# Kernel optimization log

Hardware: AMD Instinct MI355X
Metric: run time of the kernel (lower is better)

The kernel has to match this reference:

```python
import jax, jax.numpy as jnp
import numpy as np

B, NUM, LENTH, AUX = 32, 64, 64, 64
SIZE, OUT = 256, 256
IN_G = (LENTH + 1) * 2 + AUX  # 194


def _linear_params(k, fan_in, fan_out):
    # torch nn.Linear default init: U(-1/sqrt(fan_in), 1/sqrt(fan_in))
    s = 1.0 / np.sqrt(fan_in)
    kw, kb = jax.random.split(k)
    W = jax.random.uniform(kw, (fan_in, fan_out), minval=-s, maxval=s, dtype=jnp.float32)
    b = jax.random.uniform(kb, (fan_out,), minval=-s, maxval=s, dtype=jnp.float32)
    return W, b


def setup_inputs() -> dict:
    key = jax.random.key(0)
    ks = jax.random.split(key, 8)
    inp = {"x_aux": jax.random.normal(ks[0], (B, NUM, LENTH + AUX), dtype=jnp.float32)}
    dims = [("g1", IN_G, SIZE), ("g2", SIZE, SIZE), ("g3", SIZE, SIZE), ("g4", SIZE, OUT),
            ("f1", OUT, SIZE), ("f2", SIZE, SIZE), ("f3", SIZE, OUT)]
    for k, (name, fi, fo) in zip(ks[1:], dims):
        W, b = _linear_params(k, fi, fo)
        inp[name + "_w"] = W
        inp[name + "_b"] = b
    return inp


def reference(x_aux, g1_w, g1_b, g2_w, g2_b, g3_w, g3_b, g4_w, g4_b,
              f1_w, f1_b, f2_w, f2_b, f3_w, f3_b):
    bsz = x_aux.shape[0]
    # coord feature = object index i
    coord = jnp.broadcast_to(
        jnp.arange(NUM, dtype=x_aux.dtype)[None, :, None], (bsz, NUM, 1))
    x = jnp.concatenate([x_aux[:, :, :LENTH], coord], axis=-1)      # [B, N, LENTH+1]
    xa = jnp.concatenate([x_aux, coord], axis=-1)                   # [B, N, LENTH+AUX+1]
    # all-pairs broadcast+concat -> [B, N, N, IN_G]
    x_i = jnp.broadcast_to(x[:, None, :, :], (bsz, NUM, NUM, LENTH + 1))
    x_j = jnp.broadcast_to(xa[:, :, None, :], (bsz, NUM, NUM, LENTH + AUX + 1))
    pairs = jnp.concatenate([x_i, x_j], axis=-1)
    # shared g-MLP over every pair
    h = jax.nn.relu(pairs @ g1_w + g1_b)
    h = jax.nn.relu(h @ g2_w + g2_b)
    h = jax.nn.relu(h @ g3_w + g3_b)
    h = jax.nn.relu(h @ g4_w + g4_b)
    # sum-pool over all N*N pairs -> [B, OUT]
    x_g = h.sum(axis=(1, 2))
    # f-MLP (dropout treated as identity / eval mode)
    x_f = jax.nn.relu(x_g @ f1_w + f1_b)
    x_f = jax.nn.relu(x_f @ f2_w + f2_b)
    return x_f @ f3_w + f3_b
```

## Files before the change

### kernel.cpp

```cpp
#include <hip/hip_runtime.h>

#define BATCH 32
#define NOBJ  64
#define PADK  264

typedef _Float16 f16x4 __attribute__((ext_vector_type(4)));
typedef _Float16 f16x8 __attribute__((ext_vector_type(8)));
typedef float    f32x4 __attribute__((ext_vector_type(4)));
typedef float    f32x16 __attribute__((ext_vector_type(16)));

__global__ __launch_bounds__(256) void prep_weights(
    const float* __restrict__ g1w, const float* __restrict__ g2w,
    const float* __restrict__ g3w, const float* __restrict__ g4w,
    _Float16* __restrict__ wtf, float* __restrict__ xg) {
  __shared__ _Float16 tile[256][33];
  const int blk = blockIdx.x;
  const int t = threadIdx.x;
  xg[blk * 256 + t] = 0.0f;

  const int l  = blk >> 3;
  const int nt = blk & 7;
  const float* src = (l == 0) ? g1w : (l == 1) ? g2w : (l == 2) ? g3w : g4w;

  const int nn = t & 31, kb = t >> 5;
#pragma unroll 4
  for (int pass = 0; pass < 32; ++pass) {
    int kn = pass * 8 + kb;
    int ok;
    if (l == 0) {
      if (kn < 64)        ok = kn;
      else if (kn < 192)  ok = kn + 1;
      else if (kn == 192) ok = 64;
      else if (kn == 193) ok = 193;
      else                ok = -1;
    } else {
      ok = kn;
    }
    float v = (ok >= 0) ? src[(size_t)ok * 256 + nt * 32 + nn] : 0.0f;
    tile[kn][nn] = (_Float16)v;
  }
  __syncthreads();

  const int lane = t & 63;
  const int nfrag = lane & 31;
  const int kbase = (lane >> 5) * 8;
  _Float16* dst = wtf + ((size_t)(l * 8 + nt) * 16) * 512;
#pragma unroll
  for (int q = 0; q < 4; ++q) {
    int kk = (t >> 6) + 4 * q;
    f16x8 fr;
#pragma unroll
    for (int j = 0; j < 8; ++j)
      fr[j] = tile[kk * 16 + kbase + j][nfrag];
    *(f16x8*)(dst + (size_t)kk * 512 + lane * 8) = fr;
  }
}

__global__ __launch_bounds__(256, 4) void g_mlp_pool(
    const float* __restrict__ x_aux,
    const _Float16* __restrict__ wtf,
    const float* __restrict__ g1b, const float* __restrict__ g2b,
    const float* __restrict__ g3b, const float* __restrict__ g4b,
    float* __restrict__ xg) {
  __shared__ _Float16 As[64][PADK];

  const int b = blockIdx.x >> 6;
  const int i = blockIdx.x & 63;
  const int t = threadIdx.x;

  {
    const float* xb = x_aux + (size_t)b * NOBJ * 128;
    {
      const int c4 = t & 15, r0 = t >> 4;
#pragma unroll
      for (int it = 0; it < 4; ++it) {
        int r = it * 16 + r0;
        f32x4 v = *(const f32x4*)(xb + (size_t)r * 128 + c4 * 4);
        f16x4 hh = {(_Float16)v[0], (_Float16)v[1], (_Float16)v[2], (_Float16)v[3]};
        *(f16x4*)&As[r][c4 * 4] = hh;
      }
    }
    {
      const float* xi = xb + (size_t)i * 128;
      const int row = t >> 2, seg = t & 3;
#pragma unroll
      for (int u = 0; u < 4; ++u) {
        int c = seg * 32 + u * 8;
        f32x4 v0 = *(const f32x4*)(xi + c);
        f32x4 v1 = *(const f32x4*)(xi + c + 4);
        f16x8 hh = {(_Float16)v0[0], (_Float16)v0[1], (_Float16)v0[2], (_Float16)v0[3],
                    (_Float16)v1[0], (_Float16)v1[1], (_Float16)v1[2], (_Float16)v1[3]};
        *(f16x8*)&As[row][64 + c] = hh;
      }
      f16x8 z = {};
      *(f16x8*)&As[row][192 + seg * 16]     = z;
      *(f16x8*)&As[row][192 + seg * 16 + 8] = z;
      if (seg == 0) {
        As[row][192] = (_Float16)row;
        As[row][193] = (_Float16)i;
      }
    }
  }
  __syncthreads();

  const int lane = t & 63;
  const int wave = t >> 6;
  const int c31  = lane & 31;
  const int h    = lane >> 5;
  const int n0   = wave * 64;
  const float* gb[4] = {g1b, g2b, g3b, g4b};

  for (int layer = 0; layer < 4; ++layer) {
    const float bv0 = gb[layer][n0 + c31];
    const float bv1 = gb[layer][n0 + 32 + c31];

    f32x16 acc00 = {}, acc01 = {}, acc10 = {}, acc11 = {};

    const _Float16* bp0 =
        wtf + ((size_t)(layer * 8 + wave * 2) * 16) * 512 + lane * 8;
    const _Float16* bp1 = bp0 + 16 * 512;
    const _Float16* ar0 = &As[c31][h * 8];
    const _Float16* ar1 = &As[32 + c31][h * 8];

#pragma unroll
    for (int kk = 0; kk < 16; ++kk) {
      f16x8 b0 = *(const f16x8*)(bp0 + kk * 512);
      f16x8 b1 = *(const f16x8*)(bp1 + kk * 512);
      f16x8 a0 = *(const f16x8*)(ar0 + kk * 16);
      f16x8 a1 = *(const f16x8*)(ar1 + kk * 16);
      acc00 = __builtin_amdgcn_mfma_f32_32x32x16_f16(a0, b0, acc00, 0, 0, 0);
      acc10 = __builtin_amdgcn_mfma_f32_32x32x16_f16(a1, b0, acc10, 0, 0, 0);
      acc01 = __builtin_amdgcn_mfma_f32_32x32x16_f16(a0, b1, acc01, 0, 0, 0);
      acc11 = __builtin_amdgcn_mfma_f32_32x32x16_f16(a1, b1, acc11, 0, 0, 0);
    }

    if (layer < 3) {
      __syncthreads();
#pragma unroll
      for (int g = 0; g < 4; ++g)
#pragma unroll
        for (int r = 0; r < 4; ++r) {
          const int row = g * 8 + h * 4 + r;
          const int reg = g * 4 + r;
          As[row][n0 + c31]           = (_Float16)fmaxf(acc00[reg] + bv0, 0.f);
          As[32 + row][n0 + c31]      = (_Float16)fmaxf(acc10[reg] + bv0, 0.f);
          As[row][n0 + 32 + c31]      = (_Float16)fmaxf(acc01[reg] + bv1, 0.f);
          As[32 + row][n0 + 32 + c31] = (_Float16)fmaxf(acc11[reg] + bv1, 0.f);
        }
      __syncthreads();
    } else {
      float s0 = 0.f, s1 = 0.f;
#pragma unroll
      for (int reg = 0; reg < 16; ++reg) {
        s0 += fmaxf(acc00[reg] + bv0, 0.f) + fmaxf(acc10[reg] + bv0, 0.f);
        s1 += fmaxf(acc01[reg] + bv1, 0.f) + fmaxf(acc11[reg] + bv1, 0.f);
      }
      s0 += __shfl_xor(s0, 32, 64);
      s1 += __shfl_xor(s1, 32, 64);
      if (h == 0) {
        atomicAdd(&xg[b * 256 + n0 + c31], s0);
        atomicAdd(&xg[b * 256 + n0 + 32 + c31], s1);
      }
    }
  }
}

__global__ __launch_bounds__(1024) void f_mlp(
    const float* __restrict__ xg,
    const float* __restrict__ f1w, const float* __restrict__ f1b,
    const float* __restrict__ f2w, const float* __restrict__ f2b,
    const float* __restrict__ f3w, const float* __restrict__ f3b,
    float* __restrict__ out) {
  __shared__ float xs[256], ys[256], ps[4][256];
  const int b = blockIdx.x;
  const int t = threadIdx.x;
  const int n = t & 255;
  const int kc = t >> 8;

  if (t < 256) xs[t] = xg[b * 256 + t];
  __syncthreads();

  float p = 0.f;
#pragma unroll 8
  for (int k0 = 0; k0 < 64; ++k0) {
    int k = kc * 64 + k0;
    p += xs[k] * f1w[k * 256 + n];
  }
  ps[kc][n] = p;
  __syncthreads();
  if (t < 256)
    ys[t] = fmaxf(f1b[t] + ps[0][t] + ps[1][t] + ps[2][t] + ps[3][t], 0.f);
  __syncthreads();

  p = 0.f;
#pragma unroll 8
  for (int k0 = 0; k0 < 64; ++k0) {
    int k = kc * 64 + k0;
    p += ys[k] * f2w[k * 256 + n];
  }
  ps[kc][n] = p;
  __syncthreads();
  if (t < 256)
    xs[t] = fmaxf(f2b[t] + ps[0][t] + ps[1][t] + ps[2][t] + ps[3][t], 0.f);
  __syncthreads();

  p = 0.f;
#pragma unroll 8
  for (int k0 = 0; k0 < 64; ++k0) {
    int k = kc * 64 + k0;
    p += xs[k] * f3w[k * 256 + n];
  }
  ps[kc][n] = p;
  __syncthreads();
  if (t < 256)
    out[b * 256 + t] = f3b[t] + ps[0][t] + ps[1][t] + ps[2][t] + ps[3][t];
}

extern "C" void kernel_launch(void* const* d_in, const int* in_sizes, int n_in,
                              void* d_out, int out_size, void* d_ws, size_t ws_size,
                              hipStream_t stream) {
  const float* x_aux = (const float*)d_in[0];
  const float* g1w = (const float*)d_in[1];
  const float* g1b = (const float*)d_in[2];
  const float* g2w = (const float*)d_in[3];
  const float* g2b = (const float*)d_in[4];
  const float* g3w = (const float*)d_in[5];
  const float* g3b = (const float*)d_in[6];
  const float* g4w = (const float*)d_in[7];
  const float* g4b = (const float*)d_in[8];
  const float* f1w = (const float*)d_in[9];
  const float* f1b = (const float*)d_in[10];
  const float* f2w = (const float*)d_in[11];
  const float* f2b = (const float*)d_in[12];
  const float* f3w = (const float*)d_in[13];
  const float* f3b = (const float*)d_in[14];
  float* out = (float*)d_out;

  _Float16* wtf = (_Float16*)d_ws;
  float* xg = (float*)((char*)d_ws + 4u * 256u * 256u * 2u);

  hipLaunchKernelGGL(prep_weights, dim3(32), dim3(256), 0, stream,
                     g1w, g2w, g3w, g4w, wtf, xg);
  hipLaunchKernelGGL(g_mlp_pool, dim3(BATCH * NOBJ), dim3(256), 0, stream,
                     x_aux, wtf, g1b, g2b, g3b, g4b, xg);
  hipLaunchKernelGGL(f_mlp, dim3(BATCH), dim3(1024), 0, stream,
                     xg, f1w, f1b, f2w, f2b, f3w, f3b, out);
}
```

Measured before the change: 174.1 us.

## Process two object rows per block with 8 waves sharing weight fragments

Each workgroup now handles two i-values (128 pair rows) with 512 threads, and each wave computes a 128x32 output tile instead of 64x64. This halves the number of blocks and halves the global weight-fragment traffic per pair row, since each B fragment is reused across four A tiles. In exchange LDS use per block doubles to about 66KB, which limits occupancy, and the work per kernel becomes coarser, with 1024 blocks.

```diff
diff --git a/kernel.cpp b/kernel.cpp
--- a/kernel.cpp
+++ b/kernel.cpp
@@ -56,17 +56,17 @@
   }
 }
 
-__global__ __launch_bounds__(256, 4) void g_mlp_pool(
+__global__ __launch_bounds__(512, 4) void g_mlp_pool(
     const float* __restrict__ x_aux,
     const _Float16* __restrict__ wtf,
     const float* __restrict__ g1b, const float* __restrict__ g2b,
     const float* __restrict__ g3b, const float* __restrict__ g4b,
     float* __restrict__ xg) {
-  __shared__ _Float16 As[64][PADK];
-
-  const int b = blockIdx.x >> 6;
-  const int i = blockIdx.x & 63;
-  const int t = threadIdx.x;
+  __shared__ _Float16 As[128][PADK];
+
+  const int b  = blockIdx.x >> 5;
+  const int i0 = (blockIdx.x & 31) * 2;
+  const int t  = threadIdx.x;
 
   {
     const float* xb = x_aux + (size_t)b * NOBJ * 128;
@@ -74,15 +74,16 @@
       const int c4 = t & 15, r0 = t >> 4;
 #pragma unroll
       for (int it = 0; it < 4; ++it) {
-        int r = it * 16 + r0;
-        f32x4 v = *(const f32x4*)(xb + (size_t)r * 128 + c4 * 4);
+        int r = it * 32 + r0;
+        f32x4 v = *(const f32x4*)(xb + (size_t)(r & 63) * 128 + c4 * 4);
         f16x4 hh = {(_Float16)v[0], (_Float16)v[1], (_Float16)v[2], (_Float16)v[3]};
         *(f16x4*)&As[r][c4 * 4] = hh;
       }
     }
     {
-      const float* xi = xb + (size_t)i * 128;
       const int row = t >> 2, seg = t & 3;
+      const int ir = i0 + (row >> 6);
+      const float* xi = xb + (size_t)ir * 128;
 #pragma unroll
       for (int u = 0; u < 4; ++u) {
         int c = seg * 32 + u * 8;
@@ -96,8 +97,8 @@
       *(f16x8*)&As[row][192 + seg * 16]     = z;
       *(f16x8*)&As[row][192 + seg * 16 + 8] = z;
       if (seg == 0) {
-        As[row][192] = (_Float16)row;
-        As[row][193] = (_Float16)i;
+        As[row][192] = (_Float16)(row & 63);
+        As[row][193] = (_Float16)ir;
       }
     }
   }
@@ -107,31 +108,32 @@
   const int wave = t >> 6;
   const int c31  = lane & 31;
   const int h    = lane >> 5;
-  const int n0   = wave * 64;
+  const int n0   = wave * 32;
   const float* gb[4] = {g1b, g2b, g3b, g4b};
 
   for (int layer = 0; layer < 4; ++layer) {
-    const float bv0 = gb[layer][n0 + c31];
-    const float bv1 = gb[layer][n0 + 32 + c31];
-
-    f32x16 acc00 = {}, acc01 = {}, acc10 = {}, acc11 = {};
-
-    const _Float16* bp0 =
-        wtf + ((size_t)(layer * 8 + wave * 2) * 16) * 512 + lane * 8;
-    const _Float16* bp1 = bp0 + 16 * 512;
+    const float bv = gb[layer][n0 + c31];
+
+    f32x16 acc0 = {}, acc1 = {}, acc2 = {}, acc3 = {};
+
+    const _Float16* bp =
+        wtf + ((size_t)(layer * 8 + wave) * 16) * 512 + lane * 8;
     const _Float16* ar0 = &As[c31][h * 8];
     const _Float16* ar1 = &As[32 + c31][h * 8];
+    const _Float16* ar2 = &As[64 + c31][h * 8];
+    const _Float16* ar3 = &As[96 + c31][h * 8];
 
 #pragma unroll
     for (int kk = 0; kk < 16; ++kk) {
-      f16x8 b0 = *(const f16x8*)(bp0 + kk * 512);
-      f16x8 b1 = *(const f16x8*)(bp1 + kk * 512);
+      f16x8 bfr = *(const f16x8*)(bp + kk * 512);
       f16x8 a0 = *(const f16x8*)(ar0 + kk * 16);
       f16x8 a1 = *(const f16x8*)(ar1 + kk * 16);
-      acc00 = __builtin_amdgcn_mfma_f32_32x32x16_f16(a0, b0, acc00, 0, 0, 0);
-      acc10 = __builtin_amdgcn_mfma_f32_32x32x16_f16(a1, b0, acc10, 0, 0, 0);
-      acc01 = __builtin_amdgcn_mfma_f32_32x32x16_f16(a0, b1, acc01, 0, 0, 0);
-      acc11 = __builtin_amdgcn_mfma_f32_32x32x16_f16(a1, b1, acc11, 0, 0, 0);
+      f16x8 a2 = *(const f16x8*)(ar2 + kk * 16);
+      f16x8 a3 = *(const f16x8*)(ar3 + kk * 16);
+      acc0 = __builtin_amdgcn_mfma_f32_32x32x16_f16(a0, bfr, acc0, 0, 0, 0);
+      acc1 = __builtin_amdgcn_mfma_f32_32x32x16_f16(a1, bfr, acc1, 0, 0, 0);
+      acc2 = __builtin_amdgcn_mfma_f32_32x32x16_f16(a2, bfr, acc2, 0, 0, 0);
+      acc3 = __builtin_amdgcn_mfma_f32_32x32x16_f16(a3, bfr, acc3, 0, 0, 0);
     }
 
     if (layer < 3) {
@@ -142,25 +144,22 @@
         for (int r = 0; r < 4; ++r) {
           const int row = g * 8 + h * 4 + r;
           const int reg = g * 4 + r;
-          As[row][n0 + c31]           = (_Float16)fmaxf(acc00[reg] + bv0, 0.f);
-          As[32 + row][n0 + c31]      = (_Float16)fmaxf(acc10[reg] + bv0, 0.f);
-          As[row][n0 + 32 + c31]      = (_Float16)fmaxf(acc01[reg] + bv1, 0.f);
-          As[32 + row][n0 + 32 + c31] = (_Float16)fmaxf(acc11[reg] + bv1, 0.f);
+          As[row][n0 + c31]      = (_Float16)fmaxf(acc0[reg] + bv, 0.f);
+          As[32 + row][n0 + c31] = (_Float16)fmaxf(acc1[reg] + bv, 0.f);
+          As[64 + row][n0 + c31] = (_Float16)fmaxf(acc2[reg] + bv, 0.f);
+          As[96 + row][n0 + c31] = (_Float16)fmaxf(acc3[reg] + bv, 0.f);
         }
       __syncthreads();
     } else {
-      float s0 = 0.f, s1 = 0.f;
+      float s = 0.f;
 #pragma unroll
       for (int reg = 0; reg < 16; ++reg) {
-        s0 += fmaxf(acc00[reg] + bv0, 0.f) + fmaxf(acc10[reg] + bv0, 0.f);
-        s1 += fmaxf(acc01[reg] + bv1, 0.f) + fmaxf(acc11[reg] + bv1, 0.f);
-      }
-      s0 += __shfl_xor(s0, 32, 64);
-      s1 += __shfl_xor(s1, 32, 64);
-      if (h == 0) {
-        atomicAdd(&xg[b * 256 + n0 + c31], s0);
-        atomicAdd(&xg[b * 256 + n0 + 32 + c31], s1);
-      }
+        s += fmaxf(acc0[reg] + bv, 0.f) + fmaxf(acc1[reg] + bv, 0.f)
+           + fmaxf(acc2[reg] + bv, 0.f) + fmaxf(acc3[reg] + bv, 0.f);
+      }
+      s += __shfl_xor(s, 32, 64);
+      if (h == 0)
+        atomicAdd(&xg[b * 256 + n0 + c31], s);
     }
   }
 }
@@ -241,7 +240,7 @@
 
   hipLaunchKernelGGL(prep_weights, dim3(32), dim3(256), 0, stream,
                      g1w, g2w, g3w, g4w, wtf, xg);
-  hipLaunchKernelGGL(g_mlp_pool, dim3(BATCH * NOBJ), dim3(256), 0, stream,
+  hipLaunchKernelGGL(g_mlp_pool, dim3(BATCH * 32), dim3(512), 0, stream,
                      x_aux, wtf, g1b, g2b, g3b, g4b, xg);
   hipLaunchKernelGGL(f_mlp, dim3(BATCH), dim3(1024), 0, stream,
                      xg, f1w, f1b, f2w, f2b, f3w, f3b, out);
```

Result: faster. 168.9 us (-3.0%).

## Process two objects per block, prefetch B fragments, skip zero-padded K steps

Applied to the files above, without the earlier changes.

Each block now handles two i-objects (128 pair rows) with 512 threads. Two waves share each weight column slice, which halves per-block weight-fragment reuse overhead and the block count. The GEMM loop is factored into a helper that software-prefetches the next B fragment before issuing the MFMAs. The first layer runs only 13 K-steps because rows past 208 are zero padding. The larger LDS tile (128x264 halves) and bigger blocks may reduce occupancy.

```diff
diff --git a/kernel.cpp b/kernel.cpp
--- a/kernel.cpp
+++ b/kernel.cpp
@@ -8,6 +8,8 @@
 typedef _Float16 f16x8 __attribute__((ext_vector_type(8)));
 typedef float    f32x4 __attribute__((ext_vector_type(4)));
 typedef float    f32x16 __attribute__((ext_vector_type(16)));
+
+#define MFMA32(a, b, c) __builtin_amdgcn_mfma_f32_32x32x16_f16((a), (b), (c), 0, 0, 0)
 
 __global__ __launch_bounds__(256) void prep_weights(
     const float* __restrict__ g1w, const float* __restrict__ g2w,
@@ -56,17 +58,41 @@
   }
 }
 
-__global__ __launch_bounds__(256, 4) void g_mlp_pool(
+template <int STEPS>
+__device__ __forceinline__ void gemm_2x2(
+    const _Float16* bp0, const _Float16* bp1,
+    const _Float16* ar0, const _Float16* ar1,
+    f32x16& acc00, f32x16& acc10, f32x16& acc01, f32x16& acc11) {
+  f16x8 b0 = *(const f16x8*)bp0;
+  f16x8 b1 = *(const f16x8*)bp1;
+#pragma unroll
+  for (int kk = 0; kk < STEPS; ++kk) {
+    f16x8 a0 = *(const f16x8*)(ar0 + kk * 16);
+    f16x8 a1 = *(const f16x8*)(ar1 + kk * 16);
+    f16x8 nb0 = b0, nb1 = b1;
+    if (kk < STEPS - 1) {
+      nb0 = *(const f16x8*)(bp0 + (kk + 1) * 512);
+      nb1 = *(const f16x8*)(bp1 + (kk + 1) * 512);
+    }
+    acc00 = MFMA32(a0, b0, acc00);
+    acc10 = MFMA32(a1, b0, acc10);
+    acc01 = MFMA32(a0, b1, acc01);
+    acc11 = MFMA32(a1, b1, acc11);
+    b0 = nb0; b1 = nb1;
+  }
+}
+
+__global__ __launch_bounds__(512, 4) void g_mlp_pool(
     const float* __restrict__ x_aux,
     const _Float16* __restrict__ wtf,
     const float* __restrict__ g1b, const float* __restrict__ g2b,
     const float* __restrict__ g3b, const float* __restrict__ g4b,
     float* __restrict__ xg) {
-  __shared__ _Float16 As[64][PADK];
-
-  const int b = blockIdx.x >> 6;
-  const int i = blockIdx.x & 63;
-  const int t = threadIdx.x;
+  __shared__ _Float16 As[128][PADK];
+
+  const int b  = blockIdx.x >> 5;
+  const int i0 = (blockIdx.x & 31) * 2;
+  const int t  = threadIdx.x;
 
   {
     const float* xb = x_aux + (size_t)b * NOBJ * 128;
@@ -74,15 +100,16 @@
       const int c4 = t & 15, r0 = t >> 4;
 #pragma unroll
       for (int it = 0; it < 4; ++it) {
-        int r = it * 16 + r0;
-        f32x4 v = *(const f32x4*)(xb + (size_t)r * 128 + c4 * 4);
+        int r = it * 32 + r0;
+        f32x4 v = *(const f32x4*)(xb + (size_t)(r & 63) * 128 + c4 * 4);
         f16x4 hh = {(_Float16)v[0], (_Float16)v[1], (_Float16)v[2], (_Float16)v[3]};
         *(f16x4*)&As[r][c4 * 4] = hh;
       }
     }
     {
-      const float* xi = xb + (size_t)i * 128;
       const int row = t >> 2, seg = t & 3;
+      const int ir = i0 + (row >> 6);
+      const float* xi = xb + (size_t)ir * 128;
 #pragma unroll
       for (int u = 0; u < 4; ++u) {
         int c = seg * 32 + u * 8;
@@ -96,8 +123,8 @@
       *(f16x8*)&As[row][192 + seg * 16]     = z;
       *(f16x8*)&As[row][192 + seg * 16 + 8] = z;
       if (seg == 0) {
-        As[row][192] = (_Float16)row;
-        As[row][193] = (_Float16)i;
+        As[row][192] = (_Float16)(row & 63);
+        As[row][193] = (_Float16)ir;
       }
     }
   }
@@ -105,34 +132,30 @@
 
   const int lane = t & 63;
   const int wave = t >> 6;
+  const int mh   = wave & 1;
+  const int nq   = wave >> 1;
   const int c31  = lane & 31;
   const int h    = lane >> 5;
-  const int n0   = wave * 64;
+  const int n0   = nq * 64;
+  const int R    = mh * 64;
   const float* gb[4] = {g1b, g2b, g3b, g4b};
 
   for (int layer = 0; layer < 4; ++layer) {
     const float bv0 = gb[layer][n0 + c31];
     const float bv1 = gb[layer][n0 + 32 + c31];
 
-    f32x16 acc00 = {}, acc01 = {}, acc10 = {}, acc11 = {};
+    f32x16 acc00 = {}, acc10 = {}, acc01 = {}, acc11 = {};
 
     const _Float16* bp0 =
-        wtf + ((size_t)(layer * 8 + wave * 2) * 16) * 512 + lane * 8;
+        wtf + ((size_t)(layer * 8 + nq * 2) * 16) * 512 + lane * 8;
     const _Float16* bp1 = bp0 + 16 * 512;
-    const _Float16* ar0 = &As[c31][h * 8];
-    const _Float16* ar1 = &As[32 + c31][h * 8];
-
-#pragma unroll
-    for (int kk = 0; kk < 16; ++kk) {
-      f16x8 b0 = *(const f16x8*)(bp0 + kk * 512);
-      f16x8 b1 = *(const f16x8*)(bp1 + kk * 512);
-      f16x8 a0 = *(const f16x8*)(ar0 + kk * 16);
-      f16x8 a1 = *(const f16x8*)(ar1 + kk * 16);
-      acc00 = __builtin_amdgcn_mfma_f32_32x32x16_f16(a0, b0, acc00, 0, 0, 0);
-      acc10 = __builtin_amdgcn_mfma_f32_32x32x16_f16(a1, b0, acc10, 0, 0, 0);
-      acc01 = __builtin_amdgcn_mfma_f32_32x32x16_f16(a0, b1, acc01, 0, 0, 0);
-      acc11 = __builtin_amdgcn_mfma_f32_32x32x16_f16(a1, b1, acc11, 0, 0, 0);
-    }
+    const _Float16* ar0 = &As[R + c31][h * 8];
+    const _Float16* ar1 = &As[R + 32 + c31][h * 8];
+
+    if (layer == 0)
+      gemm_2x2<13>(bp0, bp1, ar0, ar1, acc00, acc10, acc01, acc11);
+    else
+      gemm_2x2<16>(bp0, bp1, ar0, ar1, acc00, acc10, acc01, acc11);
 
     if (layer < 3) {
       __syncthreads();
@@ -142,10 +165,10 @@
         for (int r = 0; r < 4; ++r) {
           const int row = g * 8 + h * 4 + r;
           const int reg = g * 4 + r;
-          As[row][n0 + c31]           = (_Float16)fmaxf(acc00[reg] + bv0, 0.f);
-          As[32 + row][n0 + c31]      = (_Float16)fmaxf(acc10[reg] + bv0, 0.f);
-          As[row][n0 + 32 + c31]      = (_Float16)fmaxf(acc01[reg] + bv1, 0.f);
-          As[32 + row][n0 + 32 + c31] = (_Float16)fmaxf(acc11[reg] + bv1, 0.f);
+          As[R + row][n0 + c31]           = (_Float16)fmaxf(acc00[reg] + bv0, 0.f);
+          As[R + 32 + row][n0 + c31]      = (_Float16)fmaxf(acc10[reg] + bv0, 0.f);
+          As[R + row][n0 + 32 + c31]      = (_Float16)fmaxf(acc01[reg] + bv1, 0.f);
+          As[R + 32 + row][n0 + 32 + c31] = (_Float16)fmaxf(acc11[reg] + bv1, 0.f);
         }
       __syncthreads();
     } else {
@@ -241,7 +264,7 @@
 
   hipLaunchKernelGGL(prep_weights, dim3(32), dim3(256), 0, stream,
                      g1w, g2w, g3w, g4w, wtf, xg);
-  hipLaunchKernelGGL(g_mlp_pool, dim3(BATCH * NOBJ), dim3(256), 0, stream,
+  hipLaunchKernelGGL(g_mlp_pool, dim3(BATCH * 32), dim3(512), 0, stream,
                      x_aux, wtf, g1b, g2b, g3b, g4b, xg);
   hipLaunchKernelGGL(f_mlp, dim3(BATCH), dim3(1024), 0, stream,
                      xg, f1w, f1b, f2w, f2b, f3w, f3b, out);
```

Result: faster. 170.3 us (-2.2%).
